# Optimization experiments

Measured on AMD Instinct MI355X. Metric: run time of the kernel, lower is better.

The kernel has to match this reference:

```python
import jax, jax.numpy as jnp
import numpy as np

BS, F, C, H, W = 2, 8, 64, 128, 128
HEADS = 4

def build_edges(bs, f):
    rows, cols, ec = [], [], 0
    for b in range(bs):
        s = b * (2 * f + 2)
        v = list(range(s, s + f)); d = list(range(s + f, s + 2 * f))
        t = s + 2 * f; g = t + 1
        for grp in (v, d, v + d, v + d, v + d + [t], [t], [g]):
            rows += grp; cols += [ec] * len(grp); ec += 1
    return np.asarray(rows, np.int32), np.asarray(cols, np.int32), ec

ROW, COL, NUM_EDGES = build_edges(BS, F)

def conv2d_s2(x, w, b):  # Conv2d k3 s2 p1 + ReLU
    y = jax.lax.conv_general_dilated(x, w, (2, 2), [(1, 1), (1, 1)],
        dimension_numbers=('NCHW', 'OIHW', 'NCHW'))
    return jax.nn.relu(y + b[None, :, None, None])

def conv_t2(x, w, b):  # ConvTranspose2d k3 s2 p1 op1 + ReLU; w: (in,out,3,3)
    wt = jnp.flip(w, (2, 3)).transpose(1, 0, 2, 3)
    y = jax.lax.conv_general_dilated(x, wt, (1, 1), [(1, 2), (1, 2)],
        lhs_dilation=(2, 2), dimension_numbers=('NCHW', 'OIHW', 'NCHW'))
    return jax.nn.relu(y + b[None, :, None, None])

def layer_norm(x, eps=1e-5):  # affine params are default ones/zeros
    mu = x.mean(-1, keepdims=True)
    var = ((x - mu) ** 2).mean(-1, keepdims=True)
    return (x - mu) / jnp.sqrt(var + eps)

def group_norm(x, groups=32, eps=1e-5):
    n, c = x.shape
    xg = x.reshape(n, groups, c // groups)
    mu = xg.mean(-1, keepdims=True)
    var = ((xg - mu) ** 2).mean(-1, keepdims=True)
    return ((xg - mu) / jnp.sqrt(var + eps)).reshape(n, c)

def se_layer(x, w1, w2):  # squeeze over node dim 0
    y = jax.nn.sigmoid(jax.nn.relu(x.mean(0) @ w1.T) @ w2.T)
    return x * y

def hypergraph_conv(x, lin_w, att, edge_w, edge_attr, out_ch):
    # PyG HypergraphConv, use_attention=True, attention_mode='node', heads=4,
    # concat=False, bias=False, eval mode (dropout inactive)
    n = x.shape[0]
    xl = (x @ lin_w.T).reshape(n, HEADS, out_ch)
    ea = (edge_attr @ lin_w.T).reshape(-1, HEADS, out_ch)
    a = (jnp.concatenate([xl[ROW], ea[COL]], axis=-1) * att).sum(-1)  # (E, heads)
    a = jax.nn.leaky_relu(a, 0.2)
    a = jnp.exp(a - jax.ops.segment_max(a, COL, num_segments=NUM_EDGES)[COL])
    a = a / (jax.ops.segment_sum(a, COL, num_segments=NUM_EDGES)[COL] + 1e-16)
    D = jax.ops.segment_sum(edge_w[COL], ROW, num_segments=n)
    D = jnp.where(D > 0, 1.0 / D, 0.0)
    B = jax.ops.segment_sum(jnp.ones(ROW.shape[0], x.dtype), COL, num_segments=NUM_EDGES)
    B = jnp.where(B > 0, 1.0 / B, 0.0)
    e = jax.ops.segment_sum(B[COL][:, None, None] * a[:, :, None] * xl[ROW], COL, num_segments=NUM_EDGES)
    o = jax.ops.segment_sum(D[ROW][:, None, None] * a[:, :, None] * e[COL], ROW, num_segments=n)
    return o.mean(1)  # concat=False -> head mean

def setup_inputs() -> dict:
    key = jax.random.key(0)
    ks = jax.random.split(key, 32)
    def n(k, shape, s=1.0):
        return jax.random.normal(k, shape, jnp.float32) * s
    def u(k, shape):
        return jax.random.uniform(k, shape, jnp.float32)
    return {
        'vision_feat': n(ks[0], (BS, F, C, H, W)), 'vision_pos': n(ks[1], (BS, F, C, H, W), 0.1),
        'motion_feat': n(ks[2], (BS, F, C, H, W)), 'motion_pos': n(ks[3], (BS, F, C, H, W), 0.1),
        'text_feat': n(ks[4], (BS, C, 16)), 'text_pos': n(ks[5], (BS, C, 16), 0.1),
        'cv1_w': n(ks[6], (2 * C, C, 3, 3), 0.04), 'cv1_b': n(ks[7], (2 * C,), 0.01),
        'cv2_w': n(ks[8], (4 * C, 2 * C, 3, 3), 0.03), 'cv2_b': n(ks[9], (4 * C,), 0.01),
        'dc1_w': n(ks[10], (2 * C, C, 3, 3), 0.04), 'dc1_b': n(ks[11], (2 * C,), 0.01),
        'dc2_w': n(ks[12], (4 * C, 2 * C, 3, 3), 0.03), 'dc2_b': n(ks[13], (4 * C,), 0.01),
        'tc1_w': n(ks[14], (4 * C, 2 * C, 3, 3), 0.03), 'tc1_b': n(ks[15], (2 * C,), 0.01),
        'tc2_w': n(ks[16], (2 * C, C, 3, 3), 0.04), 'tc2_b': n(ks[17], (C,), 0.01),
        'lin1_w': n(ks[18], (HEADS * 8 * C, 4 * C), 0.06), 'att1': n(ks[19], (1, HEADS, 16 * C), 0.05),
        'lin2_w': n(ks[20], (HEADS * 4 * C, 8 * C), 0.04), 'att2': n(ks[21], (1, HEADS, 8 * C), 0.05),
        'ew1': u(ks[22], (2 * F * BS + 2,)), 'ew2': u(ks[23], (2 * F * BS + 2,)),
        'ea1': u(ks[24], (2 * F * BS + 2, 4 * C)), 'ea2': u(ks[25], (2 * F * BS + 2, 8 * C)),
        'se1_w1': n(ks[26], (8 * C // 16, 8 * C), 0.06), 'se1_w2': n(ks[27], (8 * C, 8 * C // 16), 0.15),
        'se2_w1': n(ks[28], (4 * C // 16, 4 * C), 0.08), 'se2_w2': n(ks[29], (4 * C, 4 * C // 16), 0.2),
    }

def reference(vision_feat, vision_pos, motion_feat, motion_pos, text_feat, text_pos,
              cv1_w, cv1_b, cv2_w, cv2_b, dc1_w, dc1_b, dc2_w, dc2_b,
              tc1_w, tc1_b, tc2_w, tc2_b, lin1_w, att1, lin2_w, att2,
              ew1, ew2, ea1, ea2, se1_w1, se1_w2, se2_w1, se2_w2):
    bs, f, c, h, w = vision_feat.shape
    # text_pool: AdaptiveMaxPool1d(4) on L=16 -> exact windows of 4; view(bs,-1)
    tn = (text_feat + text_pos).reshape(bs, c, 4, 4).max(-1).reshape(bs, 4 * c)
    v0 = (vision_feat + vision_pos).reshape(bs * f, c, h, w)
    v1 = conv2d_s2(v0, cv1_w, cv1_b)          # (bs*f, 2c, h/2, w/2)
    v2 = conv2d_s2(v1, cv2_w, cv2_b)          # (bs*f, 4c, h/4, w/4)
    vn = layer_norm(v2.max((2, 3)))           # AdaptiveMaxPool2d(1) + LayerNorm
    d0 = (motion_feat + motion_pos).reshape(bs * f, c, h, w)
    dn = layer_norm(conv2d_s2(conv2d_s2(d0, dc1_w, dc1_b), dc2_w, dc2_b).max((2, 3)))
    vb = vn.reshape(bs, f, 4 * c); db = dn.reshape(bs, f, 4 * c)
    obs = tn + (vb + db).mean(1)              # observer = mean(text+v+d) over frames
    x = jnp.concatenate([vb, db, tn[:, None], obs[:, None]], axis=1).reshape(bs * (2 * f + 2), 4 * c)
    x = se_layer(group_norm(jax.nn.relu(hypergraph_conv(x, lin1_w, att1, ew1, ea1, 8 * c))), se1_w1, se1_w2)
    x = se_layer(group_norm(jax.nn.relu(hypergraph_conv(x, lin2_w, att2, ew2, ea2, 4 * c))), se2_w1, se2_w2)
    xb = x.reshape(bs, 2 * f + 2, 4 * c)
    # obs_pool: AdaptiveMaxPool1d(c) on L=4c -> windows of 4
    observers = (tn + xb[:, -1]).reshape(bs, c, 4).max(-1)
    vg = xb[:, :f].reshape(bs * f, 4 * c)
    # bilinear upsample of 1x1 == broadcast; transconv doubles size so the
    # subsequent F.interpolate calls to (h/2,w/2) and (h,w) are identities
    vr = v2 + vg[:, :, None, None]
    vr = v1 + conv_t2(vr, tc1_w, tc1_b)
    vr = v0 + conv_t2(vr, tc2_w, tc2_b)
    return vr, observers
```

## Files before the change

### kernel.cpp

```cpp
#include <hip/hip_runtime.h>
#include <hip/hip_bf16.h>
#include <cstddef>
#include <cstdint>

#define DEV_INLINE __device__ __forceinline__

typedef __attribute__((ext_vector_type(8))) short short8;
typedef __attribute__((ext_vector_type(4))) float f32x4;
typedef __attribute__((ext_vector_type(4))) unsigned short us4;

DEV_INLINE unsigned short f2bf(float f) {
  uint32_t u = __builtin_bit_cast(uint32_t, f);
  uint32_t r = (u + 0x7fffu + ((u >> 16) & 1u)) >> 16;
  return (unsigned short)r;
}
DEV_INLINE float bf2f(unsigned short u) {
  return __builtin_bit_cast(float, (uint32_t)u << 16);
}

__device__ __constant__ int c_cs[15] = {0,8,16,32,48,65,66,67,75,83,99,115,132,133,134};
__device__ __constant__ int c_row[134] = {
  0,1,2,3,4,5,6,7,
  8,9,10,11,12,13,14,15,
  0,1,2,3,4,5,6,7,8,9,10,11,12,13,14,15,
  0,1,2,3,4,5,6,7,8,9,10,11,12,13,14,15,
  0,1,2,3,4,5,6,7,8,9,10,11,12,13,14,15,16,
  16,
  17,
  18,19,20,21,22,23,24,25,
  26,27,28,29,30,31,32,33,
  18,19,20,21,22,23,24,25,26,27,28,29,30,31,32,33,
  18,19,20,21,22,23,24,25,26,27,28,29,30,31,32,33,
  18,19,20,21,22,23,24,25,26,27,28,29,30,31,32,33,34,
  34,
  35
};
__device__ __constant__ int c_col[134] = {
  0,0,0,0,0,0,0,0,
  1,1,1,1,1,1,1,1,
  2,2,2,2,2,2,2,2,2,2,2,2,2,2,2,2,
  3,3,3,3,3,3,3,3,3,3,3,3,3,3,3,3,
  4,4,4,4,4,4,4,4,4,4,4,4,4,4,4,4,4,
  5,
  6,
  7,7,7,7,7,7,7,7,
  8,8,8,8,8,8,8,8,
  9,9,9,9,9,9,9,9,9,9,9,9,9,9,9,9,
  10,10,10,10,10,10,10,10,10,10,10,10,10,10,10,10,
  11,11,11,11,11,11,11,11,11,11,11,11,11,11,11,11,11,
  12,
  13
};

__global__ void k_text_pool(const float* __restrict__ tf, const float* __restrict__ tp,
                            float* __restrict__ tn) {
  int t = blockIdx.x * blockDim.x + threadIdx.x;
  if (t >= 512) return;
  int b = t >> 8, idx = t & 255;
  int ch = idx >> 2, j = idx & 3;
  const float* p = tf + ((size_t)b * 64 + ch) * 16 + j * 4;
  const float* q = tp + ((size_t)b * 64 + ch) * 16 + j * 4;
  float m = p[0] + q[0];
  m = fmaxf(m, p[1] + q[1]);
  m = fmaxf(m, p[2] + q[2]);
  m = fmaxf(m, p[3] + q[3]);
  tn[(size_t)b * 256 + idx] = m;
}

__global__ __launch_bounds__(256) void k_prep(const float* __restrict__ a,
                                              const float* __restrict__ b,
                                              unsigned short* __restrict__ o) {
  int bid = blockIdx.x;
  int xb = bid & 1, y = (bid >> 1) & 127, n = bid >> 8;
  __shared__ unsigned int su[32][65];
  int t = threadIdx.x;
  const size_t base = ((size_t)n * 64) * 16384 + (size_t)y * 128 + xb * 64;
#pragma unroll
  for (int it = 0; it < 2; ++it) {
    int i = t + it * 256;
    int cpair = i >> 4;
    int x4 = i & 15;
    size_t off = base + (size_t)(2 * cpair) * 16384 + x4 * 4;
    float4 a0 = *reinterpret_cast<const float4*>(a + off);
    float4 b0 = *reinterpret_cast<const float4*>(b + off);
    float4 a1 = *reinterpret_cast<const float4*>(a + off + 16384);
    float4 b1 = *reinterpret_cast<const float4*>(b + off + 16384);
    unsigned int* row = &su[cpair][x4 * 4];
    row[0] = (unsigned int)f2bf(a0.x + b0.x) | ((unsigned int)f2bf(a1.x + b1.x) << 16);
    row[1] = (unsigned int)f2bf(a0.y + b0.y) | ((unsigned int)f2bf(a1.y + b1.y) << 16);
    row[2] = (unsigned int)f2bf(a0.z + b0.z) | ((unsigned int)f2bf(a1.z + b1.z) << 16);
    row[3] = (unsigned int)f2bf(a0.w + b0.w) | ((unsigned int)f2bf(a1.w + b1.w) << 16);
  }
  __syncthreads();
  unsigned int* op = (unsigned int*)(o + (((size_t)n * 128 + y) * 128 + xb * 64) * 64);
#pragma unroll
  for (int it = 0; it < 2; ++it) {
    int i = t + it * 256;
    int x = i >> 3;
    int cq = i & 7;
    uint4 v;
    v.x = su[cq * 4 + 0][x];
    v.y = su[cq * 4 + 1][x];
    v.z = su[cq * 4 + 2][x];
    v.w = su[cq * 4 + 3][x];
    *reinterpret_cast<uint4*>(op + x * 32 + cq * 4) = v;
  }
}

__global__ void k_wtrans_all(const float* __restrict__ cv1w, const float* __restrict__ dc1w,
                             const float* __restrict__ cv2w, const float* __restrict__ dc2w,
                             const float* __restrict__ tc1w, const float* __restrict__ tc2w,
                             unsigned short* __restrict__ wtb) {
  int idx = blockIdx.x * 256 + threadIdx.x;
  const float* src; int off, lci, lco; bool tra;
  if (idx < 73728)        { src = cv1w; off = 0;       lci = 6; lco = 7; tra = false; }
  else if (idx < 147456)  { src = dc1w; off = 73728;   lci = 6; lco = 7; tra = false; }
  else if (idx < 442368)  { src = cv2w; off = 147456;  lci = 7; lco = 8; tra = false; }
  else if (idx < 737280)  { src = dc2w; off = 442368;  lci = 7; lco = 8; tra = false; }
  else if (idx < 1032192) { src = tc1w; off = 737280;  lci = 8; lco = 7; tra = true;  }
  else if (idx < 1105920) { src = tc2w; off = 1032192; lci = 7; lco = 6; tra = true;  }
  else return;
  int l = idx - off;
  int ci = l & ((1 << lci) - 1);
  int r = l >> lci;
  int co = r & ((1 << lco) - 1);
  int tap = r >> lco;
  size_t si = tra ? (((size_t)ci << lco) + co) * 9 + tap
                  : (((size_t)co << lci) + ci) * 9 + tap;
  wtb[idx] = f2bf(src[si]);
}

template<int CI, int CO, int HO, int WO, int ROUT>
__global__ __launch_bounds__(512) void k_conv_mfma(
    const unsigned short* __restrict__ in,
    const unsigned short* __restrict__ wT,
    const float* __restrict__ bias,
    unsigned short* __restrict__ outn) {
  constexpr int HIN = HO * 2, WIN = WO * 2;
  constexpr int XHP = WO + 2;
  constexpr int R = 2 * ROUT + 1;
  constexpr int NPOS = R * 2 * XHP;
  constexpr int NCH = NPOS * 4;
  constexpr int NCS = CI / 32;
  constexpr int KIT = (NCH + 511) / 512;
  constexpr int CB = CO / 128;
  constexpr int OB = HO / ROUT;
  __shared__ short8 sIn[NPOS * 5];
  int bid = blockIdx.x;
  int cb = bid % CB; bid /= CB;
  int oyb = bid % OB; int n = bid / OB;
  int tid = threadIdx.x;
  int wid = tid >> 6, lane = tid & 63;
  int wm = wid >> 1, wn = wid & 1;
  int llo = lane & 15, lhi = lane >> 4;
  f32x4 acc[2][2] = {};
  const int iy0 = oyb * (2 * ROUT) - 1;
  short8 rv[KIT];
  auto loadr = [&](int cs) {
#pragma unroll
    for (int k = 0; k < KIT; ++k) {
      int i = tid + k * 512;
      short8 v = {};
      if (i < NCH) {
        int c = i & 3, q = i >> 2;
        int xh = q % XHP; int q2 = q / XHP;
        int p = q2 & 1, l = q2 >> 1;
        int x = 2 * xh + p - 1;
        int iy = iy0 + l;
        if (x >= 0 && x < WIN && iy >= 0 && iy < HIN)
          v = *reinterpret_cast<const short8*>(in + ((((size_t)n * HIN + iy) * WIN + x) * CI + cs * 32 + c * 8));
      }
      rv[k] = v;
    }
  };
  auto writes = [&]() {
#pragma unroll
    for (int k = 0; k < KIT; ++k) {
      int i = tid + k * 512;
      if (i < NCH) sIn[(i >> 2) * 5 + (i & 3)] = rv[k];
    }
  };
  loadr(0);
  for (int cs = 0; cs < NCS; ++cs) {
    writes();
    __syncthreads();
    if (cs + 1 < NCS) loadr(cs + 1);
#pragma unroll
    for (int tap = 0; tap < 9; ++tap) {
      const int ky = tap / 3, kx = tap % 3;
      short8 afr[2], bfr[2];
#pragma unroll
      for (int m = 0; m < 2; ++m) {
        int co = cb * 128 + wm * 32 + m * 16 + llo;
        afr[m] = *reinterpret_cast<const short8*>(wT + (((size_t)tap * CO + co) * CI + cs * 32 + lhi * 8));
      }
#pragma unroll
      for (int n2 = 0; n2 < 2; ++n2) {
        int pix = wn * 32 + n2 * 16 + llo;
        int oyl = (ROUT == 2) ? (pix >> 5) : 0;
        int ox = pix - oyl * WO;
        int lrow = 2 * oyl + ky;
        int pos = (lrow * 2 + (kx & 1)) * XHP + ox + (kx >> 1);
        bfr[n2] = sIn[pos * 5 + lhi];
      }
#pragma unroll
      for (int m = 0; m < 2; ++m)
#pragma unroll
        for (int n2 = 0; n2 < 2; ++n2)
          acc[m][n2] = __builtin_amdgcn_mfma_f32_16x16x32_bf16(afr[m], bfr[n2], acc[m][n2], 0, 0, 0);
    }
    __syncthreads();
  }
#pragma unroll
  for (int m = 0; m < 2; ++m) {
    int co0 = cb * 128 + wm * 32 + m * 16 + lhi * 4;
    f32x4 bv = *reinterpret_cast<const f32x4*>(bias + co0);
#pragma unroll
    for (int n2 = 0; n2 < 2; ++n2) {
      int pix = wn * 32 + n2 * 16 + llo;
      int oyl = (ROUT == 2) ? (pix >> 5) : 0;
      int ox = pix - oyl * WO;
      int oy = oyb * ROUT + oyl;
      us4 pk;
      pk[0] = f2bf(fmaxf(acc[m][n2][0] + bv[0], 0.f));
      pk[1] = f2bf(fmaxf(acc[m][n2][1] + bv[1], 0.f));
      pk[2] = f2bf(fmaxf(acc[m][n2][2] + bv[2], 0.f));
      pk[3] = f2bf(fmaxf(acc[m][n2][3] + bv[3], 0.f));
      *reinterpret_cast<us4*>(outn + ((((size_t)n * HO + oy) * WO + ox) * CO + co0)) = pk;
    }
  }
}

template<int CI, int CO, int Hi, int Wi, int QR, bool OBF, bool GADD>
__global__ __launch_bounds__(256) void k_deconv_mfma(
    const unsigned short* __restrict__ in,
    const unsigned short* __restrict__ wT,
    const float* __restrict__ bias,
    const unsigned short* __restrict__ resn,
    const float* __restrict__ gsrc,
    unsigned short* __restrict__ outn,
    float* __restrict__ outc) {
  constexpr int QC = 64 / QR;
  constexpr int WP = Wi + 1;
  constexpr int NPOS = (QR + 1) * WP;
  constexpr int NCH = NPOS * 4;
  constexpr int NCS = CI / 32;
  constexpr int KIT = (NCH + 255) / 256;
  constexpr int CB = CO / 64;
  constexpr int OB = Hi / QR;
  constexpr int Ho = Hi * 2, Wo = Wi * 2;
  __shared__ short8 sIn[NPOS * 5];
  int bid = blockIdx.x;
  int cb = bid % CB; bid /= CB;
  int oyb = bid % OB; int n = bid / OB;
  int tid = threadIdx.x;
  int wid = tid >> 6, lane = tid & 63;
  int wm = wid >> 1, wn = wid & 1;
  int llo = lane & 15, lhi = lane >> 4;
  int qy0 = oyb * QR;
  const float* g = nullptr;
  if constexpr (GADD) g = gsrc + ((size_t)((n >> 3) * 18 + (n & 7))) * 256;
  f32x4 acc[4][2][2] = {};
  constexpr int tap_p[9] = {3,2,3,1,0,1,3,2,3};
  constexpr int tap_b[9] = {3,2,2,1,0,0,1,0,0};
  short8 rv[KIT];
  auto loadr = [&](int cs) {
#pragma unroll
    for (int k = 0; k < KIT; ++k) {
      int i = tid + k * 256;
      short8 v = {};
      if (i < NCH) {
        int c = i & 3, q = i >> 2;
        int x = q % WP, l = q / WP;
        int iy = qy0 + l;
        if (x < Wi && iy < Hi) {
          v = *reinterpret_cast<const short8*>(in + (((size_t)(n * Hi + iy) * Wi + x) * CI + cs * 32 + c * 8));
          if constexpr (GADD) {
#pragma unroll
            for (int j = 0; j < 8; ++j) {
              float fv = bf2f((unsigned short)v[j]) + g[cs * 32 + c * 8 + j];
              v[j] = (short)f2bf(fv);
            }
          }
        }
      }
      rv[k] = v;
    }
  };
  auto writes = [&]() {
#pragma unroll
    for (int k = 0; k < KIT; ++k) {
      int i = tid + k * 256;
      if (i < NCH) sIn[(i >> 2) * 5 + (i & 3)] = rv[k];
    }
  };
  loadr(0);
  for (int cs = 0; cs < NCS; ++cs) {
    writes();
    __syncthreads();
    if (cs + 1 < NCS) loadr(cs + 1);
    short8 bfr[2][4];
#pragma unroll
    for (int n2 = 0; n2 < 2; ++n2) {
      int pix = wn * 32 + n2 * 16 + llo;
      int qyl = pix / QC, qx = pix % QC;
#pragma unroll
      for (int bs = 0; bs < 4; ++bs) {
        int pos = (qyl + (bs >> 1)) * WP + qx + (bs & 1);
        bfr[n2][bs] = sIn[pos * 5 + lhi];
      }
    }
#pragma unroll
    for (int tap = 0; tap < 9; ++tap) {
      short8 afr[2];
#pragma unroll
      for (int m = 0; m < 2; ++m) {
        int co = cb * 64 + wm * 32 + m * 16 + llo;
        afr[m] = *reinterpret_cast<const short8*>(wT + (((size_t)tap * CO + co) * CI + cs * 32 + lhi * 8));
      }
#pragma unroll
      for (int m = 0; m < 2; ++m)
#pragma unroll
        for (int n2 = 0; n2 < 2; ++n2)
          acc[tap_p[tap]][m][n2] = __builtin_amdgcn_mfma_f32_16x16x32_bf16(
              afr[m], bfr[n2][tap_b[tap]], acc[tap_p[tap]][m][n2], 0, 0, 0);
    }
    __syncthreads();
  }
#pragma unroll
  for (int m = 0; m < 2; ++m) {
    int co0 = cb * 64 + wm * 32 + m * 16 + lhi * 4;
    f32x4 bv = *reinterpret_cast<const f32x4*>(bias + co0);
#pragma unroll
    for (int n2 = 0; n2 < 2; ++n2) {
      int pix = wn * 32 + n2 * 16 + llo;
      int qyl = pix / QC, qx = pix % QC;
      int qy = qy0 + qyl;
      if constexpr (OBF) {
#pragma unroll
        for (int p = 0; p < 4; ++p) {
          int oy = 2 * qy + (p >> 1);
          int ox = 2 * qx + (p & 1);
          size_t ad = ((size_t)(n * Ho + oy) * Wo + ox) * CO + co0;
          us4 r = *reinterpret_cast<const us4*>(resn + ad);
          us4 pk;
#pragma unroll
          for (int c = 0; c < 4; ++c)
            pk[c] = f2bf(bf2f(r[c]) + fmaxf(acc[p][m][n2][c] + bv[c], 0.f));
          *reinterpret_cast<us4*>(outn + ad) = pk;
        }
      } else {
        int qx2 = 2 * qx;
#pragma unroll
        for (int dy = 0; dy < 2; ++dy) {
          int oy = 2 * qy + dy;
          size_t rb = ((size_t)(n * Ho + oy) * Wo + qx2) * CO + co0;
          us4 r0 = *reinterpret_cast<const us4*>(resn + rb);
          us4 r1 = *reinterpret_cast<const us4*>(resn + rb + CO);
#pragma unroll
          for (int c = 0; c < 4; ++c) {
            float2 st;
            st.x = bf2f(r0[c]) + fmaxf(acc[dy * 2][m][n2][c] + bv[c], 0.f);
            st.y = bf2f(r1[c]) + fmaxf(acc[dy * 2 + 1][m][n2][c] + bv[c], 0.f);
            *reinterpret_cast<float2*>(outc + ((size_t)(n * CO + co0 + c) * Ho + oy) * Wo + qx2) = st;
          }
        }
      }
    }
  }
}

__global__ __launch_bounds__(256) void k_max_part(const unsigned short* __restrict__ x,
                                                  float* __restrict__ pmax) {
  int n = blockIdx.x >> 3, pg = blockIdx.x & 7;
  int t = threadIdx.x;
  int c8 = t & 31;
  int ps = t >> 5;
  const unsigned short* base = x + (size_t)n * 262144 + (size_t)pg * 32768 + (size_t)c8 * 8;
  float m[8];
#pragma unroll
  for (int j = 0; j < 8; ++j) m[j] = -1e30f;
  for (int p = ps * 16; p < ps * 16 + 16; ++p) {
    short8 v = *reinterpret_cast<const short8*>(base + (size_t)p * 256);
#pragma unroll
    for (int j = 0; j < 8; ++j) m[j] = fmaxf(m[j], bf2f((unsigned short)v[j]));
  }
  __shared__ float sred[8][264];
#pragma unroll
  for (int j = 0; j < 8; ++j) sred[ps][c8 * 8 + j] = m[j];
  __syncthreads();
  float mm = sred[0][t];
#pragma unroll
  for (int g = 1; g < 8; ++g) mm = fmaxf(mm, sred[g][t]);
  pmax[((size_t)n * 8 + pg) * 256 + t] = mm;
}

__global__ __launch_bounds__(256) void k_ln(const float* __restrict__ pmax,
                                            float* __restrict__ out) {
  int n = blockIdx.x, ch = threadIdx.x;
  float m = -1e30f;
#pragma unroll
  for (int g = 0; g < 8; ++g)
    m = fmaxf(m, pmax[((size_t)n * 8 + g) * 256 + ch]);
  __shared__ float r1[256], r2[256];
  r1[ch] = m; __syncthreads();
  for (int s = 128; s > 0; s >>= 1) { if (ch < s) r1[ch] += r1[ch + s]; __syncthreads(); }
  float mu = r1[0] * (1.f / 256.f);
  float d = m - mu;
  r2[ch] = d * d; __syncthreads();
  for (int s = 128; s > 0; s >>= 1) { if (ch < s) r2[ch] += r2[ch + s]; __syncthreads(); }
  out[(size_t)n * 256 + ch] = d * rsqrtf(r2[0] * (1.f / 256.f) + 1e-5f);
}

__global__ void k_build_x(const float* __restrict__ vn, const float* __restrict__ dn,
                          const float* __restrict__ tn, float* __restrict__ x0) {
  int b = blockIdx.x, ch = threadIdx.x;
  float s = 0.f;
  for (int f = 0; f < 8; ++f) {
    float vv = vn[((size_t)b * 8 + f) * 256 + ch];
    float dd = dn[((size_t)b * 8 + f) * 256 + ch];
    s += vv + dd;
    x0[((size_t)b * 18 + f) * 256 + ch] = vv;
    x0[((size_t)b * 18 + 8 + f) * 256 + ch] = dd;
  }
  float tv = tn[(size_t)b * 256 + ch];
  x0[((size_t)b * 18 + 16) * 256 + ch] = tv;
  x0[((size_t)b * 18 + 17) * 256 + ch] = tv + s * (1.f / 8.f);
}

__global__ __launch_bounds__(256) void k_gnn_lin(
    const float* __restrict__ x, const float* __restrict__ ea,
    const float* __restrict__ w, float* __restrict__ y, int K, int M) {
  int chunks = M >> 8;
  int r = blockIdx.x / chunks;
  int ob = (blockIdx.x % chunks) * 256 + threadIdx.x;
  const float* src = (r < 36) ? (x + (size_t)r * K) : (ea + (size_t)(r - 36) * K);
  __shared__ __align__(16) float sxr[512];
  for (int k = threadIdx.x; k < K; k += 256) sxr[k] = src[k];
  __syncthreads();
  const float4* w4 = reinterpret_cast<const float4*>(w + (size_t)ob * K);
  const float4* x4 = reinterpret_cast<const float4*>(sxr);
  float acc = 0.f;
  int k4 = K >> 2;
  for (int k = 0; k < k4; ++k) {
    float4 a = x4[k], b = w4[k];
    acc += a.x * b.x + a.y * b.y + a.z * b.z + a.w * b.w;
  }
  y[(size_t)r * M + ob] = acc;
}

template<int OC>
__global__ __launch_bounds__(256) void k_gnn_attsm(
    const float* __restrict__ y, const float* __restrict__ att,
    float* __restrict__ attw) {
  int t = threadIdx.x;
  __shared__ float sx_s[144], seb_s[60];
  __shared__ float a_s[536];
  if (t < 200) {
    int r = t >> 2, h = t & 3;
    const float4* row = reinterpret_cast<const float4*>(y + ((size_t)r * 4 + h) * OC);
    const float4* ar = reinterpret_cast<const float4*>(att + (size_t)h * 2 * OC + (r < 36 ? 0 : OC));
    float s = 0.f;
#pragma unroll 4
    for (int k = 0; k < OC / 4; ++k) {
      float4 a = row[k], b = ar[k];
      s += a.x * b.x + a.y * b.y + a.z * b.z + a.w * b.w;
    }
    if (r < 36) sx_s[r * 4 + h] = s; else seb_s[(r - 36) * 4 + h] = s;
  }
  __syncthreads();
  for (int idx = t; idx < 536; idx += 256) {
    int i = idx >> 2, h = idx & 3;
    float v = sx_s[c_row[i] * 4 + h] + seb_s[c_col[i] * 4 + h];
    a_s[idx] = (v > 0.f) ? v : 0.2f * v;
  }
  __syncthreads();
  if (t < 56) {
    int c = t >> 2, h = t & 3;
    int st = c_cs[c], en = c_cs[c + 1];
    float m = -1e30f;
    for (int i = st; i < en; ++i) m = fmaxf(m, a_s[i * 4 + h]);
    float s = 0.f;
    for (int i = st; i < en; ++i) { float e = __expf(a_s[i * 4 + h] - m); a_s[i * 4 + h] = e; s += e; }
    float inv = 1.f / (s + 1e-16f);
    for (int i = st; i < en; ++i) a_s[i * 4 + h] *= inv;
  }
  __syncthreads();
  for (int idx = t; idx < 536; idx += 256) attw[idx] = a_s[idx];
}

template<int OC>
__global__ __launch_bounds__(256) void k_edge_agg(
    const float* __restrict__ y, const float* __restrict__ attw,
    float* __restrict__ eb) {
  int idx = blockIdx.x * 256 + threadIdx.x;
  if (idx >= 14 * 4 * OC) return;
  int ch = idx % OC;
  int h = (idx / OC) & 3;
  int c = idx / (4 * OC);
  int st = c_cs[c], en = c_cs[c + 1];
  float s = 0.f;
  for (int i = st; i < en; ++i)
    s += attw[i * 4 + h] * y[(size_t)c_row[i] * (4 * OC) + h * OC + ch];
  eb[idx] = s * (1.f / (float)(en - st));
}

template<int OC>
__global__ __launch_bounds__(256) void k_node_agg(
    const float* __restrict__ attw, const float* __restrict__ eb,
    const float* __restrict__ ew, float* __restrict__ ho) {
  int idx = blockIdx.x * 256 + threadIdx.x;
  if (idx >= 36 * OC) return;
  int ch = idx % OC;
  int node = idx / OC;
  int b = node / 18, ln = node % 18;
  int ncols, cols[4], gis[4];
  if (ln < 16) {
    ncols = 4;
    cols[0] = b * 7 + (ln < 8 ? 0 : 1); gis[0] = b * 67 + ln;
    cols[1] = b * 7 + 2; gis[1] = b * 67 + 16 + ln;
    cols[2] = b * 7 + 3; gis[2] = b * 67 + 32 + ln;
    cols[3] = b * 7 + 4; gis[3] = b * 67 + 48 + ln;
  } else if (ln == 16) {
    ncols = 2;
    cols[0] = b * 7 + 4; gis[0] = b * 67 + 64;
    cols[1] = b * 7 + 5; gis[1] = b * 67 + 65;
    cols[2] = cols[3] = 0; gis[2] = gis[3] = 0;
  } else {
    ncols = 1;
    cols[0] = b * 7 + 6; gis[0] = b * 67 + 66;
    cols[1] = cols[2] = cols[3] = 0; gis[1] = gis[2] = gis[3] = 0;
  }
  float dsum = 0.f;
#pragma unroll
  for (int k = 0; k < 4; ++k) if (k < ncols) dsum += ew[cols[k]];
  float D = dsum > 0.f ? 1.f / dsum : 0.f;
  float s = 0.f;
#pragma unroll
  for (int k = 0; k < 4; ++k) {
    if (k < ncols) {
#pragma unroll
      for (int h = 0; h < 4; ++h)
        s += attw[gis[k] * 4 + h] * eb[((size_t)cols[k] * 4 + h) * OC + ch];
    }
  }
  ho[idx] = fmaxf(0.25f * D * s, 0.f);
}

template<int C, int Cr>
__global__ __launch_bounds__(512) void k_gn_se(
    const float* __restrict__ hin, const float* __restrict__ w1,
    const float* __restrict__ w2, float* __restrict__ x) {
  int t = threadIdx.x;
  constexpr int gs = C >> 5;
  for (int idx = t; idx < 36 * 32; idx += 512) {
    int node = idx >> 5, g = idx & 31;
    const float* p = hin + (size_t)node * C + g * gs;
    float s = 0.f, s2 = 0.f;
#pragma unroll
    for (int k = 0; k < gs; ++k) { float v = p[k]; s += v; s2 += v * v; }
    float mu = s * (1.f / gs);
    float var = s2 * (1.f / gs) - mu * mu;
    float inv = rsqrtf(fmaxf(var, 0.f) + 1e-5f);
    float* q = x + (size_t)node * C + g * gs;
#pragma unroll
    for (int k = 0; k < gs; ++k) q[k] = (p[k] - mu) * inv;
  }
  __threadfence_block();
  __syncthreads();
  __shared__ float smean[C];
  __shared__ float spart[Cr][17];
  __shared__ float shid[Cr];
  __shared__ float sscale[C];
  if (t < C) {
    float s = 0.f;
    for (int nn = 0; nn < 36; ++nn) s += x[(size_t)nn * C + t];
    smean[t] = s * (1.f / 36.f);
  }
  __syncthreads();
  if (t < Cr * 16) {
    int hid = t >> 4, sub = t & 15;
    constexpr int CH = C / 16;
    float s = 0.f;
#pragma unroll
    for (int k = 0; k < CH; ++k)
      s += w1[(size_t)hid * C + sub * CH + k] * smean[sub * CH + k];
    spart[hid][sub] = s;
  }
  __syncthreads();
  if (t < Cr) {
    float s = 0.f;
#pragma unroll
    for (int k = 0; k < 16; ++k) s += spart[t][k];
    shid[t] = fmaxf(s, 0.f);
  }
  __syncthreads();
  if (t < C) {
    float s = 0.f;
#pragma unroll
    for (int k = 0; k < Cr; ++k) s += w2[(size_t)t * Cr + k] * shid[k];
    sscale[t] = 1.f / (1.f + __expf(-s));
  }
  __syncthreads();
  for (int idx = t; idx < 36 * C; idx += 512) x[idx] *= sscale[idx % C];
}

__global__ void k_obs(const float* __restrict__ tn, const float* __restrict__ x2,
                      float* __restrict__ out) {
  int t = threadIdx.x;
  if (t >= 128) return;
  int b = t >> 6, ch = t & 63;
  const float* a = tn + (size_t)b * 256 + ch * 4;
  const float* c = x2 + ((size_t)b * 18 + 17) * 256 + ch * 4;
  float m = a[0] + c[0];
  m = fmaxf(m, a[1] + c[1]);
  m = fmaxf(m, a[2] + c[2]);
  m = fmaxf(m, a[3] + c[3]);
  out[b * 64 + ch] = m;
}

extern "C" void kernel_launch(void* const* d_in, const int* in_sizes, int n_in,
                              void* d_out, int out_size, void* d_ws, size_t ws_size,
                              hipStream_t stream) {
  (void)in_sizes; (void)n_in; (void)out_size; (void)ws_size;
  const float* vf    = (const float*)d_in[0];
  const float* vp    = (const float*)d_in[1];
  const float* mf    = (const float*)d_in[2];
  const float* mp    = (const float*)d_in[3];
  const float* tf    = (const float*)d_in[4];
  const float* tp    = (const float*)d_in[5];
  const float* cv1w  = (const float*)d_in[6];
  const float* cv1b  = (const float*)d_in[7];
  const float* cv2w  = (const float*)d_in[8];
  const float* cv2b  = (const float*)d_in[9];
  const float* dc1w  = (const float*)d_in[10];
  const float* dc1b  = (const float*)d_in[11];
  const float* dc2w  = (const float*)d_in[12];
  const float* dc2b  = (const float*)d_in[13];
  const float* tc1w  = (const float*)d_in[14];
  const float* tc1b  = (const float*)d_in[15];
  const float* tc2w  = (const float*)d_in[16];
  const float* tc2b  = (const float*)d_in[17];
  const float* lin1w = (const float*)d_in[18];
  const float* att1  = (const float*)d_in[19];
  const float* lin2w = (const float*)d_in[20];
  const float* att2  = (const float*)d_in[21];
  const float* ew1   = (const float*)d_in[22];
  const float* ew2   = (const float*)d_in[23];
  const float* ea1   = (const float*)d_in[24];
  const float* ea2   = (const float*)d_in[25];
  const float* se1w1 = (const float*)d_in[26];
  const float* se1w2 = (const float*)d_in[27];
  const float* se2w1 = (const float*)d_in[28];
  const float* se2w2 = (const float*)d_in[29];

  float* ws  = (float*)d_ws;
  float* out = (float*)d_out;

  unsigned short* p0n = (unsigned short*)(ws);
  unsigned short* q1n = (unsigned short*)(ws + 8388608);
  unsigned short* t1n = (unsigned short*)(ws + 12582912);
  unsigned short* v2n = (unsigned short*)(ws + 16777216);
  unsigned short* wtb = (unsigned short*)(ws + 18874368);
  float* sm   = ws + 19427328;
  float* tn   = sm;
  float* vn   = sm + 512;
  float* dn   = sm + 4608;
  float* x0   = sm + 8704;
  float* xl   = sm + 17920;
  float* eb   = sm + 120520;
  float* ho   = sm + 149192;
  float* x1   = sm + 167624;
  float* x2   = sm + 186056;
  float* attw = sm + 195272;
  float* pmax = sm + 195904;

  unsigned short* wTc1 = wtb;
  unsigned short* wTd1 = wtb + 73728;
  unsigned short* wTc2 = wtb + 147456;
  unsigned short* wTd2 = wtb + 442368;
  unsigned short* wTt1 = wtb + 737280;
  unsigned short* wTt2 = wtb + 1032192;

  k_wtrans_all<<<4320, 256, 0, stream>>>(cv1w, dc1w, cv2w, dc2w, tc1w, tc2w, wtb);

  k_text_pool<<<2, 256, 0, stream>>>(tf, tp, tn);

  k_prep<<<4096, 256, 0, stream>>>(mf, mp, p0n);
  k_conv_mfma<64, 128, 64, 64, 1><<<1024, 512, 0, stream>>>(p0n, wTd1, dc1b, q1n);
  k_conv_mfma<128, 256, 32, 32, 2><<<512, 512, 0, stream>>>(q1n, wTd2, dc2b, v2n);
  k_max_part<<<128, 256, 0, stream>>>(v2n, pmax);
  k_ln<<<16, 256, 0, stream>>>(pmax, dn);

  k_prep<<<4096, 256, 0, stream>>>(vf, vp, p0n);
  k_conv_mfma<64, 128, 64, 64, 1><<<1024, 512, 0, stream>>>(p0n, wTc1, cv1b, q1n);
  k_conv_mfma<128, 256, 32, 32, 2><<<512, 512, 0, stream>>>(q1n, wTc2, cv2b, v2n);
  k_max_part<<<128, 256, 0, stream>>>(v2n, pmax);
  k_ln<<<16, 256, 0, stream>>>(pmax, vn);

  k_build_x<<<2, 256, 0, stream>>>(vn, dn, tn, x0);

  k_gnn_lin<<<50 * 8, 256, 0, stream>>>(x0, ea1, lin1w, xl, 256, 2048);
  k_gnn_attsm<512><<<1, 256, 0, stream>>>(xl, att1, attw);
  k_edge_agg<512><<<112, 256, 0, stream>>>(xl, attw, eb);
  k_node_agg<512><<<72, 256, 0, stream>>>(attw, eb, ew1, ho);
  k_gn_se<512, 32><<<1, 512, 0, stream>>>(ho, se1w1, se1w2, x1);

  k_gnn_lin<<<50 * 4, 256, 0, stream>>>(x1, ea2, lin2w, xl, 512, 1024);
  k_gnn_attsm<256><<<1, 256, 0, stream>>>(xl, att2, attw);
  k_edge_agg<256><<<56, 256, 0, stream>>>(xl, attw, eb);
  k_node_agg<256><<<36, 256, 0, stream>>>(attw, eb, ew2, ho);
  k_gn_se<256, 16><<<1, 512, 0, stream>>>(ho, se2w1, se2w2, x2);

  k_obs<<<1, 128, 0, stream>>>(tn, x2, out + 16777216);

  k_deconv_mfma<256, 128, 32, 32, 2, true, true><<<512, 256, 0, stream>>>(
      v2n, wTt1, tc1b, q1n, x2, t1n, nullptr);
  k_deconv_mfma<128, 64, 64, 64, 1, false, false><<<1024, 256, 0, stream>>>(
      t1n, wTt2, tc2b, p0n, nullptr, nullptr, out);
}
```

Baseline: 486.6 us.

## Batch weight-fragment loads, add occupancy hints, fuse text pool, nontemporal stores

Several unrelated tweaks land together. The conv and deconv MFMA kernels now load all nine taps' weight fragments before the MFMA loop so global-load latency overlaps, and both kernels get a min-blocks-per-CU launch bound of 3. k_prep issues all its global loads before converting and storing to shared memory, the final deconv output uses nontemporal stores, and the text pooling kernel is folded into k_build_x to drop one launch. Holding more fragments in registers raises register pressure, which the occupancy hint may force into spills.

```diff
diff --git a/kernel.cpp b/kernel.cpp
--- a/kernel.cpp
+++ b/kernel.cpp
@@ -7,6 +7,7 @@
 
 typedef __attribute__((ext_vector_type(8))) short short8;
 typedef __attribute__((ext_vector_type(4))) float f32x4;
+typedef __attribute__((ext_vector_type(2))) float f32x2;
 typedef __attribute__((ext_vector_type(4))) unsigned short us4;
 
 DEV_INLINE unsigned short f2bf(float f) {
@@ -52,21 +53,6 @@
   13
 };
 
-__global__ void k_text_pool(const float* __restrict__ tf, const float* __restrict__ tp,
-                            float* __restrict__ tn) {
-  int t = blockIdx.x * blockDim.x + threadIdx.x;
-  if (t >= 512) return;
-  int b = t >> 8, idx = t & 255;
-  int ch = idx >> 2, j = idx & 3;
-  const float* p = tf + ((size_t)b * 64 + ch) * 16 + j * 4;
-  const float* q = tp + ((size_t)b * 64 + ch) * 16 + j * 4;
-  float m = p[0] + q[0];
-  m = fmaxf(m, p[1] + q[1]);
-  m = fmaxf(m, p[2] + q[2]);
-  m = fmaxf(m, p[3] + q[3]);
-  tn[(size_t)b * 256 + idx] = m;
-}
-
 __global__ __launch_bounds__(256) void k_prep(const float* __restrict__ a,
                                               const float* __restrict__ b,
                                               unsigned short* __restrict__ o) {
@@ -75,29 +61,33 @@
   __shared__ unsigned int su[32][65];
   int t = threadIdx.x;
   const size_t base = ((size_t)n * 64) * 16384 + (size_t)y * 128 + xb * 64;
+  float4 A0[2], B0[2], A1[2], B1[2];
 #pragma unroll
   for (int it = 0; it < 2; ++it) {
     int i = t + it * 256;
-    int cpair = i >> 4;
-    int x4 = i & 15;
+    int cpair = i >> 4, x4 = i & 15;
     size_t off = base + (size_t)(2 * cpair) * 16384 + x4 * 4;
-    float4 a0 = *reinterpret_cast<const float4*>(a + off);
-    float4 b0 = *reinterpret_cast<const float4*>(b + off);
-    float4 a1 = *reinterpret_cast<const float4*>(a + off + 16384);
-    float4 b1 = *reinterpret_cast<const float4*>(b + off + 16384);
-    unsigned int* row = &su[cpair][x4 * 4];
-    row[0] = (unsigned int)f2bf(a0.x + b0.x) | ((unsigned int)f2bf(a1.x + b1.x) << 16);
-    row[1] = (unsigned int)f2bf(a0.y + b0.y) | ((unsigned int)f2bf(a1.y + b1.y) << 16);
-    row[2] = (unsigned int)f2bf(a0.z + b0.z) | ((unsigned int)f2bf(a1.z + b1.z) << 16);
-    row[3] = (unsigned int)f2bf(a0.w + b0.w) | ((unsigned int)f2bf(a1.w + b1.w) << 16);
-  }
-  __syncthreads();
-  unsigned int* op = (unsigned int*)(o + (((size_t)n * 128 + y) * 128 + xb * 64) * 64);
+    A0[it] = *reinterpret_cast<const float4*>(a + off);
+    B0[it] = *reinterpret_cast<const float4*>(b + off);
+    A1[it] = *reinterpret_cast<const float4*>(a + off + 16384);
+    B1[it] = *reinterpret_cast<const float4*>(b + off + 16384);
+  }
 #pragma unroll
   for (int it = 0; it < 2; ++it) {
     int i = t + it * 256;
-    int x = i >> 3;
-    int cq = i & 7;
+    int cpair = i >> 4, x4 = i & 15;
+    unsigned int* row = &su[cpair][x4 * 4];
+    row[0] = (unsigned int)f2bf(A0[it].x + B0[it].x) | ((unsigned int)f2bf(A1[it].x + B1[it].x) << 16);
+    row[1] = (unsigned int)f2bf(A0[it].y + B0[it].y) | ((unsigned int)f2bf(A1[it].y + B1[it].y) << 16);
+    row[2] = (unsigned int)f2bf(A0[it].z + B0[it].z) | ((unsigned int)f2bf(A1[it].z + B1[it].z) << 16);
+    row[3] = (unsigned int)f2bf(A0[it].w + B0[it].w) | ((unsigned int)f2bf(A1[it].w + B1[it].w) << 16);
+  }
+  __syncthreads();
+  unsigned int* op = (unsigned int*)(o + (((size_t)n * 128 + y) * 128 + xb * 64) * 64);
+#pragma unroll
+  for (int it = 0; it < 2; ++it) {
+    int i = t + it * 256;
+    int x = i >> 3, cq = i & 7;
     uint4 v;
     v.x = su[cq * 4 + 0][x];
     v.y = su[cq * 4 + 1][x];
@@ -131,7 +121,7 @@
 }
 
 template<int CI, int CO, int HO, int WO, int ROUT>
-__global__ __launch_bounds__(512) void k_conv_mfma(
+__global__ __launch_bounds__(512, 3) void k_conv_mfma(
     const unsigned short* __restrict__ in,
     const unsigned short* __restrict__ wT,
     const float* __restrict__ bias,
@@ -185,15 +175,18 @@
     writes();
     __syncthreads();
     if (cs + 1 < NCS) loadr(cs + 1);
+    short8 afr9[9][2];
+#pragma unroll
+    for (int tap = 0; tap < 9; ++tap)
+#pragma unroll
+      for (int m = 0; m < 2; ++m) {
+        int co = cb * 128 + wm * 32 + m * 16 + llo;
+        afr9[tap][m] = *reinterpret_cast<const short8*>(wT + (((size_t)tap * CO + co) * CI + cs * 32 + lhi * 8));
+      }
 #pragma unroll
     for (int tap = 0; tap < 9; ++tap) {
       const int ky = tap / 3, kx = tap % 3;
-      short8 afr[2], bfr[2];
-#pragma unroll
-      for (int m = 0; m < 2; ++m) {
-        int co = cb * 128 + wm * 32 + m * 16 + llo;
-        afr[m] = *reinterpret_cast<const short8*>(wT + (((size_t)tap * CO + co) * CI + cs * 32 + lhi * 8));
-      }
+      short8 bfr[2];
 #pragma unroll
       for (int n2 = 0; n2 < 2; ++n2) {
         int pix = wn * 32 + n2 * 16 + llo;
@@ -207,7 +200,7 @@
       for (int m = 0; m < 2; ++m)
 #pragma unroll
         for (int n2 = 0; n2 < 2; ++n2)
-          acc[m][n2] = __builtin_amdgcn_mfma_f32_16x16x32_bf16(afr[m], bfr[n2], acc[m][n2], 0, 0, 0);
+          acc[m][n2] = __builtin_amdgcn_mfma_f32_16x16x32_bf16(afr9[tap][m], bfr[n2], acc[m][n2], 0, 0, 0);
     }
     __syncthreads();
   }
@@ -232,7 +225,7 @@
 }
 
 template<int CI, int CO, int Hi, int Wi, int QR, bool OBF, bool GADD>
-__global__ __launch_bounds__(256) void k_deconv_mfma(
+__global__ __launch_bounds__(256, 3) void k_deconv_mfma(
     const unsigned short* __restrict__ in,
     const unsigned short* __restrict__ wT,
     const float* __restrict__ bias,
@@ -311,19 +304,19 @@
       }
     }
 #pragma unroll
-    for (int tap = 0; tap < 9; ++tap) {
-      short8 afr[2];
-#pragma unroll
-      for (int m = 0; m < 2; ++m) {
+    for (int m = 0; m < 2; ++m) {
+      short8 afr9[9];
+#pragma unroll
+      for (int tap = 0; tap < 9; ++tap) {
         int co = cb * 64 + wm * 32 + m * 16 + llo;
-        afr[m] = *reinterpret_cast<const short8*>(wT + (((size_t)tap * CO + co) * CI + cs * 32 + lhi * 8));
+        afr9[tap] = *reinterpret_cast<const short8*>(wT + (((size_t)tap * CO + co) * CI + cs * 32 + lhi * 8));
       }
 #pragma unroll
-      for (int m = 0; m < 2; ++m)
+      for (int tap = 0; tap < 9; ++tap)
 #pragma unroll
         for (int n2 = 0; n2 < 2; ++n2)
           acc[tap_p[tap]][m][n2] = __builtin_amdgcn_mfma_f32_16x16x32_bf16(
-              afr[m], bfr[n2][tap_b[tap]], acc[tap_p[tap]][m][n2], 0, 0, 0);
+              afr9[tap], bfr[n2][tap_b[tap]], acc[tap_p[tap]][m][n2], 0, 0, 0);
     }
     __syncthreads();
   }
@@ -359,10 +352,11 @@
           us4 r1 = *reinterpret_cast<const us4*>(resn + rb + CO);
 #pragma unroll
           for (int c = 0; c < 4; ++c) {
-            float2 st;
-            st.x = bf2f(r0[c]) + fmaxf(acc[dy * 2][m][n2][c] + bv[c], 0.f);
-            st.y = bf2f(r1[c]) + fmaxf(acc[dy * 2 + 1][m][n2][c] + bv[c], 0.f);
-            *reinterpret_cast<float2*>(outc + ((size_t)(n * CO + co0 + c) * Ho + oy) * Wo + qx2) = st;
+            f32x2 st;
+            st[0] = bf2f(r0[c]) + fmaxf(acc[dy * 2][m][n2][c] + bv[c], 0.f);
+            st[1] = bf2f(r1[c]) + fmaxf(acc[dy * 2 + 1][m][n2][c] + bv[c], 0.f);
+            __builtin_nontemporal_store(st,
+                reinterpret_cast<f32x2*>(outc + ((size_t)(n * CO + co0 + c) * Ho + oy) * Wo + qx2));
           }
         }
       }
@@ -412,9 +406,18 @@
   out[(size_t)n * 256 + ch] = d * rsqrtf(r2[0] * (1.f / 256.f) + 1e-5f);
 }
 
-__global__ void k_build_x(const float* __restrict__ vn, const float* __restrict__ dn,
-                          const float* __restrict__ tn, float* __restrict__ x0) {
+__global__ void k_build_x(const float* __restrict__ tf, const float* __restrict__ tp,
+                          const float* __restrict__ vn, const float* __restrict__ dn,
+                          float* __restrict__ tn, float* __restrict__ x0) {
   int b = blockIdx.x, ch = threadIdx.x;
+  int c4 = ch >> 2, j = ch & 3;
+  const float* p = tf + ((size_t)b * 64 + c4) * 16 + j * 4;
+  const float* q = tp + ((size_t)b * 64 + c4) * 16 + j * 4;
+  float tv = p[0] + q[0];
+  tv = fmaxf(tv, p[1] + q[1]);
+  tv = fmaxf(tv, p[2] + q[2]);
+  tv = fmaxf(tv, p[3] + q[3]);
+  tn[(size_t)b * 256 + ch] = tv;
   float s = 0.f;
   for (int f = 0; f < 8; ++f) {
     float vv = vn[((size_t)b * 8 + f) * 256 + ch];
@@ -423,7 +426,6 @@
     x0[((size_t)b * 18 + f) * 256 + ch] = vv;
     x0[((size_t)b * 18 + 8 + f) * 256 + ch] = dd;
   }
-  float tv = tn[(size_t)b * 256 + ch];
   x0[((size_t)b * 18 + 16) * 256 + ch] = tv;
   x0[((size_t)b * 18 + 17) * 256 + ch] = tv + s * (1.f / 8.f);
 }
@@ -684,8 +686,6 @@
 
   k_wtrans_all<<<4320, 256, 0, stream>>>(cv1w, dc1w, cv2w, dc2w, tc1w, tc2w, wtb);
 
-  k_text_pool<<<2, 256, 0, stream>>>(tf, tp, tn);
-
   k_prep<<<4096, 256, 0, stream>>>(mf, mp, p0n);
   k_conv_mfma<64, 128, 64, 64, 1><<<1024, 512, 0, stream>>>(p0n, wTd1, dc1b, q1n);
   k_conv_mfma<128, 256, 32, 32, 2><<<512, 512, 0, stream>>>(q1n, wTd2, dc2b, v2n);
@@ -698,7 +698,7 @@
   k_max_part<<<128, 256, 0, stream>>>(v2n, pmax);
   k_ln<<<16, 256, 0, stream>>>(pmax, vn);
 
-  k_build_x<<<2, 256, 0, stream>>>(vn, dn, tn, x0);
+  k_build_x<<<2, 256, 0, stream>>>(tf, tp, vn, dn, tn, x0);
 
   k_gnn_lin<<<50 * 8, 256, 0, stream>>>(x0, ea1, lin1w, xl, 256, 2048);
   k_gnn_attsm<512><<<1, 256, 0, stream>>>(xl, att1, attw);
```

After: 482.7 us. About the same (-0.8%).
